# Kernel optimization log

Measured on AMD Instinct MI355X. Metric: run time of the kernel, lower is better.

Reference implementation:

```python
import jax, jax.numpy as jnp
import numpy as np
import math

EMB = 64
NEG_INF = -1e30

def _layernorm(x, g, b, eps=1e-5):
    mu = jnp.mean(x, axis=-1, keepdims=True)
    var = jnp.mean((x - mu) ** 2, axis=-1, keepdims=True)
    return (x - mu) * jax.lax.rsqrt(var + eps) * g + b

def setup_inputs() -> dict:
    key = jax.random.key(0)
    ks = jax.random.split(key, 8)
    b, t, n, d = 16, 12, 307, EMB
    s = 1.0 / math.sqrt(d)
    inp = {
        'x': jax.random.normal(ks[0], (b, t, n, d), dtype=jnp.float32),
        'stg': jax.random.uniform(ks[1], (b, n, t, n), dtype=jnp.float32),
        'topk': 3,
        'q_w': jax.random.normal(ks[2], (d, d), dtype=jnp.float32) * s,
        'q_b': jnp.zeros((d,), jnp.float32),
        'k_w': jax.random.normal(ks[3], (d, d), dtype=jnp.float32) * s,
        'k_b': jnp.zeros((d,), jnp.float32),
        'ln_g': jnp.ones((d,), jnp.float32),
        'ln_b': jnp.zeros((d,), jnp.float32),
        'ffn_ln_g': jnp.ones((d,), jnp.float32),
        'ffn_ln_b': jnp.zeros((d,), jnp.float32),
        'fc1_w': jax.random.normal(ks[4], (4 * d, d), dtype=jnp.float32) * s,
        'fc1_b': jnp.zeros((4 * d,), jnp.float32),
        'fc2_w': jax.random.normal(ks[5], (d, 4 * d), dtype=jnp.float32) * (0.5 * s),
        'fc2_b': jnp.zeros((d,), jnp.float32),
    }
    return inp

def reference(x, stg, topk, q_w, q_b, k_w, k_b, ln_g, ln_b, ffn_ln_g, ffn_ln_b, fc1_w, fc1_b, fc2_w, fc2_b):
    b, t, n, d = x.shape
    scale = 1.0 / math.sqrt(d)
    x_ = _layernorm(x, ln_g, ln_b)           # [b,t,n,d]
    y_ = x_[:, -1]                            # [b,n,d] last timestep
    q = y_ @ q_w.T + q_b                      # [b,n,d]
    k = x_ @ k_w.T + k_b                      # [b,t,n,d]
    dg = jnp.einsum('bnd,btmd->bntm', q, k) * scale
    sag = jax.nn.sigmoid(dg) * stg * scale    # gated scores [b,n,t,n]
    sag = sag.reshape(b, n, t * n)
    if topk > 0:
        kk = topk * n if topk < 5 else topk   # mirrors torch's self.topk *= n
        top_values, _ = jax.lax.top_k(sag, kk)
        thr = top_values[..., -1:]
        sag = jnp.where(sag > thr, sag, NEG_INF)  # strict >, as in torch code
    sag = jax.nn.softmax(sag, axis=-1).reshape(b, n, t, n)  # dropout in eval mode = identity
    o = jnp.einsum('bntm,btmd->bnd', sag, x_)
    h = o + y_
    # FFN: pre-norm residual MLP (LayerNorm -> Linear(d,4d) -> ReLU -> Linear(4d,d) + residual)
    z = _layernorm(h, ffn_ln_g, ffn_ln_b)
    z = jax.nn.relu(z @ fc1_w.T + fc1_b) @ fc2_w.T + fc2_b
    return h + z
```

## Files before the change

### kernel.cpp

```cpp
#include <hip/hip_runtime.h>

typedef __bf16 bf16x8 __attribute__((ext_vector_type(8)));
typedef float  f32x4  __attribute__((ext_vector_type(4)));
typedef unsigned short u16x8 __attribute__((ext_vector_type(8)));
typedef unsigned short u16x4 __attribute__((ext_vector_type(4)));

constexpr int BB    = 16;
constexpr int TT    = 12;
constexpr int NN    = 307;
constexpr int TN    = TT * NN;
constexpr int ROWSX = BB * TT * NN;
constexpr int ROWSH = BB * NN;
constexpr int SST1  = 3712;
constexpr int SSTR  = 3840;
constexpr int HPS   = ROWSH * 64;
constexpr int KQ    = 928;
constexpr int WBS   = 152;
constexpr float SCALE = 0.125f;

__device__ __forceinline__ float wred_sum(float v) {
#pragma unroll
    for (int m = 32; m > 0; m >>= 1) v += __shfl_xor(v, m, 64);
    return v;
}

__global__ __launch_bounds__(256) void prep_k(const float* __restrict__ qw,
                                              const float* __restrict__ qb,
                                              const float* __restrict__ kw,
                                              const float* __restrict__ kb,
                                              const float* __restrict__ fc1w,
                                              const float* __restrict__ fc2w,
                                              const float* __restrict__ x,
                                              const float* __restrict__ g,
                                              const float* __restrict__ b,
                                              float* __restrict__ M,
                                              float* __restrict__ b2,
                                              float* __restrict__ vv,
                                              float* __restrict__ cc,
                                              __bf16* __restrict__ fc1b16,
                                              __bf16* __restrict__ fc2b16,
                                              __bf16* __restrict__ xnb,
                                              float* __restrict__ y32) {
    int bx = blockIdx.x, t = threadIdx.x;
    int w = t >> 6, lane = t & 63;
    if (bx < 16) {
        int e = bx * 4 + w, d = lane;
        float acc = 0.f;
        for (int dp = 0; dp < 64; ++dp) acc += qw[dp * 64 + e] * kw[dp * 64 + d];
        M[e * 64 + d] = acc;
        float vp = wred_sum(qw[d * 64 + e] * kb[d]);
        if (lane == 0) vv[e] = vp;
        if (e == 0) {
            float bv = 0.f;
            for (int dp = 0; dp < 64; ++dp) bv += qb[dp] * kw[dp * 64 + d];
            b2[d] = bv;
            float cp = wred_sum(qb[d] * kb[d]);
            if (d == 0) *cc = cp;
        }
    } else if (bx < 144) {
        int i = (bx - 16) * 256 + t;
        if (i < 16384) fc1b16[i] = (__bf16)fc1w[i];
        else fc2b16[i - 16384] = (__bf16)fc2w[i - 16384];
    } else {
        int r = (bx - 144) * 4 + w;
        if (r >= ROWSX) return;
        float val = x[r * 64 + lane];
        float mu  = wred_sum(val) * (1.f / 64.f);
        float dv  = val - mu;
        float var = wred_sum(dv * dv) * (1.f / 64.f);
        float xv  = dv * rsqrtf(var + 1e-5f) * g[lane] + b[lane];
        xnb[(size_t)r * 64 + lane] = (__bf16)xv;
        int tt = (r / NN) % TT;
        if (tt == TT - 1) {
            int bbv = r / (NN * TT), n = r % NN;
            y32[(bbv * NN + n) * 64 + lane] = xv;
        }
    }
}

__global__ __launch_bounds__(256) void tq_k(const __bf16* __restrict__ xnb,
                                            __bf16* __restrict__ xnT,
                                            const float* __restrict__ y32,
                                            const float* __restrict__ M,
                                            const float* __restrict__ b2,
                                            const float* __restrict__ vv,
                                            const float* __restrict__ ccp,
                                            __bf16* __restrict__ qtb,
                                            float* __restrict__ cq) {
    __shared__ unsigned short tile[64][65];
    int bx = blockIdx.x, t = threadIdx.x;
    if (bx < 928) {
        int bb = bx / 58, j0 = (bx % 58) * 64;
        const unsigned short* src = (const unsigned short*)xnb;
        unsigned short* dst = (unsigned short*)xnT;
#pragma unroll
        for (int i = 0; i < 16; ++i) {
            int f = t + 256 * i, jr = f >> 6, dc = f & 63;
            int j = j0 + jr;
            tile[jr][dc] = (j < TN) ? src[((size_t)bb * TN + j) * 64 + dc] : (unsigned short)0;
        }
        __syncthreads();
#pragma unroll
        for (int i = 0; i < 16; ++i) {
            int f = t + 256 * i, d = f >> 6, jj = f & 63;
            dst[((size_t)bb * 64 + d) * SSTR + j0 + jj] = tile[jj][d];
        }
    } else {
        int w = t >> 6, l = t & 63;
        int rr = (bx - 928) * 4 + w;
        if (rr >= ROWSH) return;
        float y = y32[rr * 64 + l];
        float acc = b2[l];
#pragma unroll
        for (int e = 0; e < 64; ++e) acc += __shfl(y, e, 64) * M[e * 64 + l];
        qtb[(size_t)rr * 64 + l] = (__bf16)acc;
        float cp = wred_sum(y * vv[l]);
        if (l == 0) cq[rr] = cp + *ccp;
    }
}

__global__ __launch_bounds__(256, 4) void score_k(const __bf16* __restrict__ qtb,
                                                  const float* __restrict__ cq,
                                                  const __bf16* __restrict__ xnb,
                                                  const float* __restrict__ stg,
                                                  __bf16* __restrict__ sag) {
    __shared__ unsigned short wb[64 * WBS];
    int bb = blockIdx.z, n0 = blockIdx.y * 64, j0 = blockIdx.x * 128;
    int t = threadIdx.x;
    int w = t >> 6, lane = t & 63;
    int m16 = lane & 15, q4 = lane >> 4;

    const float* stgb = stg + (size_t)bb * NN * TN;
    float4 sv[4][2];
    float cn[4];
#pragma unroll
    for (int nt = 0; nt < 4; ++nt) {
        int n = n0 + nt * 16 + m16;
        const float* srow = stgb + (size_t)min(n, NN - 1) * TN;
#pragma unroll
        for (int jj = 0; jj < 2; ++jj) {
            int jb = j0 + (w * 2 + jj) * 16 + q4 * 4;
            float4 s4 = {0.f, 0.f, 0.f, 0.f};
            if (jb < TN) s4 = *(const float4*)(srow + jb);
            sv[nt][jj] = s4;
        }
        cn[nt] = (n < NN) ? cq[bb * NN + n] : 0.f;
    }

    bf16x8 a[2][2];
#pragma unroll
    for (int jj = 0; jj < 2; ++jj) {
        const bf16x8* ap = (const bf16x8*)(xnb + ((size_t)bb * TN + j0 + (w * 2 + jj) * 16 + m16) * 64);
        a[jj][0] = ap[q4];
        a[jj][1] = ap[q4 + 4];
    }

    f32x4 acc[2][4];
#pragma unroll
    for (int nt = 0; nt < 4; ++nt) {
        const bf16x8* bp = (const bf16x8*)(qtb + ((size_t)bb * NN + n0 + nt * 16 + m16) * 64);
        bf16x8 b0 = bp[q4], b1 = bp[q4 + 4];
#pragma unroll
        for (int jj = 0; jj < 2; ++jj) {
            f32x4 c = {0.f, 0.f, 0.f, 0.f};
            c = __builtin_amdgcn_mfma_f32_16x16x32_bf16(a[jj][0], b0, c, 0, 0, 0);
            c = __builtin_amdgcn_mfma_f32_16x16x32_bf16(a[jj][1], b1, c, 0, 0, 0);
            acc[jj][nt] = c;
        }
    }

#pragma unroll
    for (int nt = 0; nt < 4; ++nt) {
#pragma unroll
        for (int jj = 0; jj < 2; ++jj) {
            int jb = j0 + (w * 2 + jj) * 16 + q4 * 4;
            float svv[4] = {sv[nt][jj].x, sv[nt][jj].y, sv[nt][jj].z, sv[nt][jj].w};
            u16x4 hw;
#pragma unroll
            for (int r = 0; r < 4; ++r) {
                float dg = (acc[jj][nt][r] + cn[nt]) * SCALE;
                float s  = 1.f / (1.f + __expf(-dg));
                float wv = (jb + r < TN) ? s * svv[r] * SCALE : 0.f;
                __bf16 wb16 = (__bf16)wv;
                hw[r] = *(unsigned short*)&wb16;
            }
            *(u16x4*)&wb[(nt * 16 + m16) * WBS + (w * 2 + jj) * 16 + q4 * 4] = hw;
        }
    }
    __syncthreads();

#pragma unroll
    for (int i = 0; i < 4; ++i) {
        int chunk = t + i * 256;
        int row = chunk >> 4, c8 = (chunk & 15) * 8;
        int n = n0 + row;
        if (n < NN) {
            u16x8 v = *(const u16x8*)&wb[row * WBS + c8];
            *(u16x8*)((unsigned short*)sag + (size_t)(bb * NN + n) * SST1 + j0 + c8) = v;
        }
    }
}

__global__ __launch_bounds__(256) void smax_k(__bf16* __restrict__ sagB,
                                              const int* __restrict__ topk_p,
                                              float* __restrict__ rsum) {
    int t = threadIdx.x;
    int wid = t >> 6, lane = t & 63;
    int row = blockIdx.x * 4 + wid;
    if (row >= ROWSH) return;

    int topkv = *topk_p;
    bool selAll = (topkv <= 0);
    int kk = 0;
    if (!selAll) {
        kk = (topkv < 5) ? topkv * NN : topkv;
        if (kk > TN) kk = TN;
    }

    u16x8* src = (u16x8*)((unsigned short*)sagB + (size_t)row * SST1);
    u16x8 va[8];
#pragma unroll
    for (int ci = 0; ci < 8; ++ci) {
        int c = lane + (ci << 6);
        u16x8 v = {0, 0, 0, 0, 0, 0, 0, 0};
        if (c < 464) v = src[c];
        va[ci] = v;
    }
    int vmb = 0;
#pragma unroll
    for (int ci = 0; ci < 8; ++ci)
#pragma unroll
        for (int e = 0; e < 8; ++e) vmb = max(vmb, (int)va[ci][e]);
#pragma unroll
    for (int m = 32; m > 0; m >>= 1) vmb = max(vmb, __shfl_xor(vmb, m, 64));
    float vmax = __uint_as_float(((unsigned)vmb) << 16);

    unsigned thrb = 0;
    if (!selAll) {
        unsigned lo = 0, hi = (unsigned)vmb;
        while (lo < hi) {
            unsigned mid = (lo + hi) >> 1;
            int cnt = 0;
#pragma unroll
            for (int ci = 0; ci < 8; ++ci)
#pragma unroll
                for (int e = 0; e < 8; ++e)
                    cnt += (int)__popcll(__ballot((unsigned)va[ci][e] > mid));
            if (cnt < kk) hi = mid; else lo = mid + 1;
        }
        thrb = lo;
    }

    float local = 0.f;
#pragma unroll
    for (int ci = 0; ci < 8; ++ci) {
        int c = lane + (ci << 6);
        int nvv = (c < 460) ? 8 : ((c == 460) ? 4 : 0);
#pragma unroll
        for (int e = 0; e < 8; ++e) {
            unsigned u = va[ci][e];
            bool sel = selAll ? (e < nvv) : (u > thrb);
            float ev = sel ? __expf(__uint_as_float(u << 16) - vmax) : 0.f;
            local += ev;
            __bf16 eb = (__bf16)ev;
            va[ci][e] = *(unsigned short*)&eb;
        }
    }
    local = wred_sum(local);
    bool uni = !(local > 0.f);
    if (lane == 0) rsum[row] = uni ? (float)TN : local;

    if (uni) {
        __bf16 one = (__bf16)1.f, zero = (__bf16)0.f;
#pragma unroll
        for (int ci = 0; ci < 8; ++ci) {
            int c = lane + (ci << 6);
            if (c < 464) {
                int nvv = (c < 460) ? 8 : ((c == 460) ? 4 : 0);
                bf16x8 o;
#pragma unroll
                for (int e = 0; e < 8; ++e) o[e] = (e < nvv) ? one : zero;
                *(bf16x8*)&src[c] = o;
            }
        }
    } else {
#pragma unroll
        for (int ci = 0; ci < 8; ++ci) {
            int c = lane + (ci << 6);
            if (c < 464) src[c] = va[ci];
        }
    }
}

__global__ __launch_bounds__(256) void pv_k(const __bf16* __restrict__ sagB,
                                            const __bf16* __restrict__ xnT,
                                            const float* __restrict__ y32,
                                            const float* __restrict__ rsum,
                                            float* __restrict__ hp) {
    int bb = blockIdx.z, kq = blockIdx.y, n0 = blockIdx.x * 16;
    int wid = threadIdx.x >> 6, lane = threadIdx.x & 63;
    int m16 = lane & 15, q4 = lane >> 4;

    int arow = min(n0 + m16, NN - 1);
    const __bf16* ab  = sagB + (size_t)(bb * NN + arow) * SST1 + kq * KQ + q4 * 8;
    const __bf16* bbp = xnT + ((size_t)bb * 64 + wid * 16 + m16) * SSTR + kq * KQ + q4 * 8;

    f32x4 acc0 = {0.f, 0.f, 0.f, 0.f}, acc1 = {0.f, 0.f, 0.f, 0.f};
#pragma unroll 4
    for (int ks = 0; ks < 29; ++ks) {
        bf16x8 a = *(const bf16x8*)(ab + ks * 32);
        bf16x8 b = *(const bf16x8*)(bbp + ks * 32);
        if (ks & 1) acc1 = __builtin_amdgcn_mfma_f32_16x16x32_bf16(a, b, acc1, 0, 0, 0);
        else        acc0 = __builtin_amdgcn_mfma_f32_16x16x32_bf16(a, b, acc0, 0, 0, 0);
    }
#pragma unroll
    for (int r = 0; r < 4; ++r) {
        int n = n0 + q4 * 4 + r;
        if (n < NN) {
            size_t o = (size_t)(bb * NN + n) * 64 + wid * 16 + m16;
            float inv = 1.f / rsum[bb * NN + n];
            float v = (acc0[r] + acc1[r]) * inv;
            if (kq == 0) v += y32[o];
            hp[(size_t)kq * HPS + o] = v;
        }
    }
}

__global__ __launch_bounds__(256) void ffn_k(const float* __restrict__ hp,
                                             const float* __restrict__ g,
                                             const float* __restrict__ bln,
                                             const __bf16* __restrict__ fc1b16,
                                             const float* __restrict__ fc1b,
                                             const __bf16* __restrict__ fc2b16,
                                             const float* __restrict__ fc2b,
                                             float* __restrict__ out) {
    __shared__ __bf16 zb[16 * 68];
    __shared__ __bf16 ab[16 * 264];
    __shared__ float hs[16][66];
    int t = threadIdx.x, r0 = blockIdx.x * 16;
    int wid = t >> 6, lane = t & 63;
    int m16 = lane & 15, q4 = lane >> 4;

#pragma unroll
    for (int q = 0; q < 4; ++q) {
        int rl = wid * 4 + q;
        size_t i = (size_t)(r0 + rl) * 64 + lane;
        float val = hp[i] + hp[HPS + i] + hp[2 * HPS + i] + hp[3 * HPS + i];
        hs[rl][lane] = val;
        float mu  = wred_sum(val) * (1.f / 64.f);
        float dv  = val - mu;
        float var = wred_sum(dv * dv) * (1.f / 64.f);
        zb[rl * 68 + lane] = (__bf16)(dv * rsqrtf(var + 1e-5f) * g[lane] + bln[lane]);
    }
    __syncthreads();

    bf16x8 a0 = *(const bf16x8*)&zb[m16 * 68 + q4 * 8];
    bf16x8 a1 = *(const bf16x8*)&zb[m16 * 68 + 32 + q4 * 8];
#pragma unroll
    for (int jt2 = 0; jt2 < 4; ++jt2) {
        int j0t = (wid * 4 + jt2) * 16;
        const __bf16* bp = fc1b16 + (size_t)(j0t + m16) * 64 + q4 * 8;
        f32x4 c = {0.f, 0.f, 0.f, 0.f};
        c = __builtin_amdgcn_mfma_f32_16x16x32_bf16(a0, *(const bf16x8*)bp, c, 0, 0, 0);
        c = __builtin_amdgcn_mfma_f32_16x16x32_bf16(a1, *(const bf16x8*)(bp + 32), c, 0, 0, 0);
        int j = j0t + m16;
        float bias = fc1b[j];
#pragma unroll
        for (int r = 0; r < 4; ++r)
            ab[(q4 * 4 + r) * 264 + j] = (__bf16)fmaxf(c[r] + bias, 0.f);
    }
    __syncthreads();

    f32x4 c2a = {0.f, 0.f, 0.f, 0.f}, c2b = {0.f, 0.f, 0.f, 0.f};
    const __bf16* b2p = fc2b16 + (size_t)(wid * 16 + m16) * 256 + q4 * 8;
#pragma unroll
    for (int k8 = 0; k8 < 8; k8 += 2) {
        bf16x8 aa0 = *(const bf16x8*)&ab[m16 * 264 + k8 * 32 + q4 * 8];
        bf16x8 aa1 = *(const bf16x8*)&ab[m16 * 264 + (k8 + 1) * 32 + q4 * 8];
        c2a = __builtin_amdgcn_mfma_f32_16x16x32_bf16(aa0, *(const bf16x8*)(b2p + k8 * 32), c2a, 0, 0, 0);
        c2b = __builtin_amdgcn_mfma_f32_16x16x32_bf16(aa1, *(const bf16x8*)(b2p + (k8 + 1) * 32), c2b, 0, 0, 0);
    }
    int d = wid * 16 + m16;
    float bias2 = fc2b[d];
#pragma unroll
    for (int r = 0; r < 4; ++r) {
        size_t row = (size_t)(r0 + q4 * 4 + r);
        size_t o = row * 64 + d;
        out[o] = hs[q4 * 4 + r][d] + c2a[r] + c2b[r] + bias2;
    }
}

extern "C" void kernel_launch(void* const* d_in, const int* in_sizes, int n_in,
                              void* d_out, int out_size, void* d_ws, size_t ws_size,
                              hipStream_t stream) {
    const float* x    = (const float*)d_in[0];
    const float* stg  = (const float*)d_in[1];
    const int*   topk = (const int*)d_in[2];
    const float* qw   = (const float*)d_in[3];
    const float* qb   = (const float*)d_in[4];
    const float* kw   = (const float*)d_in[5];
    const float* kb   = (const float*)d_in[6];
    const float* lng  = (const float*)d_in[7];
    const float* lnb  = (const float*)d_in[8];
    const float* flng = (const float*)d_in[9];
    const float* flnb = (const float*)d_in[10];
    const float* fc1w = (const float*)d_in[11];
    const float* fc1b = (const float*)d_in[12];
    const float* fc2w = (const float*)d_in[13];
    const float* fc2b = (const float*)d_in[14];
    float* out = (float*)d_out;

    float* ws = (float*)d_ws;
    __bf16* xnb = (__bf16*)ws;
    float* p1   = ws + 1886208;
    __bf16* xnT = (__bf16*)p1;
    float* p2   = p1 + 1966080;
    __bf16* qtb = (__bf16*)p2;
    float* y32  = p2 + 157696;
    float* cq   = y32 + 314368;
    float* M    = cq + 4928;
    float* b2   = M + 4096;
    float* vv   = b2 + 64;
    float* cc   = vv + 64;
    __bf16* fc1b16 = (__bf16*)(cc + 16);
    __bf16* fc2b16 = (__bf16*)((float*)fc1b16 + 8192);
    __bf16* sag = (__bf16*)((float*)fc2b16 + 8192);
    float* hp   = (float*)sag + 9116672;
    float* rsum = hp + 4 * HPS;

    prep_k<<<144 + (ROWSX + 3) / 4, 256, 0, stream>>>(qw, qb, kw, kb, fc1w, fc2w,
                                                      x, lng, lnb,
                                                      M, b2, vv, cc,
                                                      fc1b16, fc2b16, xnb, y32);
    tq_k<<<928 + (ROWSH + 3) / 4, 256, 0, stream>>>(xnb, xnT, y32, M, b2, vv, cc, qtb, cq);
    score_k<<<dim3((TN + 127) / 128, (NN + 63) / 64, BB), 256, 0, stream>>>(qtb, cq, xnb, stg, sag);
    smax_k<<<(ROWSH + 3) / 4, 256, 0, stream>>>(sag, topk, rsum);
    pv_k<<<dim3((NN + 15) / 16, 4, BB), 256, 0, stream>>>(sag, xnT, y32, rsum, hp);
    ffn_k<<<ROWSH / 16, 256, 0, stream>>>(hp, flng, flnb, fc1b16, fc1b, fc2b16, fc2b, out);
}
```

Baseline: 245.8 us.

## Move transpose into score kernel and swizzle pv block order

Splits the old transpose+q kernel: the small q projection runs alone, and the xnb→xnT transpose blocks are appended to the score kernel's 1D grid so they run alongside score tiles. Separately, pv_k remaps block indices with an 8-way interleave, likely to spread batches and k-chunks across XCDs for better L2 locality. This trades a lighter serial q kernel and overlapping work against added index arithmetic and shared LDS reuse in score_k.

```diff
diff --git a/kernel.cpp b/kernel.cpp
--- a/kernel.cpp
+++ b/kernel.cpp
@@ -16,6 +16,7 @@
 constexpr int HPS   = ROWSH * 64;
 constexpr int KQ    = 928;
 constexpr int WBS   = 152;
+constexpr int SCORE_VB = 145 * BB;
 constexpr float SCALE = 0.125f;
 
 __device__ __forceinline__ float wred_sum(float v) {
@@ -78,19 +79,39 @@
     }
 }
 
-__global__ __launch_bounds__(256) void tq_k(const __bf16* __restrict__ xnb,
-                                            __bf16* __restrict__ xnT,
-                                            const float* __restrict__ y32,
+__global__ __launch_bounds__(256) void qt_k(const float* __restrict__ y32,
                                             const float* __restrict__ M,
                                             const float* __restrict__ b2,
                                             const float* __restrict__ vv,
                                             const float* __restrict__ ccp,
                                             __bf16* __restrict__ qtb,
                                             float* __restrict__ cq) {
-    __shared__ unsigned short tile[64][65];
-    int bx = blockIdx.x, t = threadIdx.x;
-    if (bx < 928) {
-        int bb = bx / 58, j0 = (bx % 58) * 64;
+    int w = threadIdx.x >> 6, l = threadIdx.x & 63;
+    int rr = blockIdx.x * 4 + w;
+    if (rr >= ROWSH) return;
+    float y = y32[rr * 64 + l];
+    float acc = b2[l];
+#pragma unroll
+    for (int e = 0; e < 64; ++e) acc += __shfl(y, e, 64) * M[e * 64 + l];
+    qtb[(size_t)rr * 64 + l] = (__bf16)acc;
+    float cp = wred_sum(y * vv[l]);
+    if (l == 0) cq[rr] = cp + *ccp;
+}
+
+__global__ __launch_bounds__(256, 4) void score_k(const __bf16* __restrict__ qtb,
+                                                  const float* __restrict__ cq,
+                                                  const __bf16* __restrict__ xnb,
+                                                  const float* __restrict__ stg,
+                                                  __bf16* __restrict__ sag,
+                                                  __bf16* __restrict__ xnT) {
+    __shared__ unsigned short wb[64 * WBS];
+    int vb = blockIdx.x;
+    int t = threadIdx.x;
+
+    if (vb >= SCORE_VB) {
+        int u = vb - SCORE_VB;
+        int bb = u / 58, j0 = (u % 58) * 64;
+        unsigned short (*tile)[65] = (unsigned short(*)[65])wb;
         const unsigned short* src = (const unsigned short*)xnb;
         unsigned short* dst = (unsigned short*)xnT;
 #pragma unroll
@@ -105,28 +126,11 @@
             int f = t + 256 * i, d = f >> 6, jj = f & 63;
             dst[((size_t)bb * 64 + d) * SSTR + j0 + jj] = tile[jj][d];
         }
-    } else {
-        int w = t >> 6, l = t & 63;
-        int rr = (bx - 928) * 4 + w;
-        if (rr >= ROWSH) return;
-        float y = y32[rr * 64 + l];
-        float acc = b2[l];
-#pragma unroll
-        for (int e = 0; e < 64; ++e) acc += __shfl(y, e, 64) * M[e * 64 + l];
-        qtb[(size_t)rr * 64 + l] = (__bf16)acc;
-        float cp = wred_sum(y * vv[l]);
-        if (l == 0) cq[rr] = cp + *ccp;
-    }
-}
-
-__global__ __launch_bounds__(256, 4) void score_k(const __bf16* __restrict__ qtb,
-                                                  const float* __restrict__ cq,
-                                                  const __bf16* __restrict__ xnb,
-                                                  const float* __restrict__ stg,
-                                                  __bf16* __restrict__ sag) {
-    __shared__ unsigned short wb[64 * WBS];
-    int bb = blockIdx.z, n0 = blockIdx.y * 64, j0 = blockIdx.x * 128;
-    int t = threadIdx.x;
+        return;
+    }
+
+    int jb = vb % 29, nb = (vb / 29) % 5, bb = vb / 145;
+    int n0 = nb * 64, j0 = jb * 128;
     int w = t >> 6, lane = t & 63;
     int m16 = lane & 15, q4 = lane >> 4;
 
@@ -139,9 +143,9 @@
         const float* srow = stgb + (size_t)min(n, NN - 1) * TN;
 #pragma unroll
         for (int jj = 0; jj < 2; ++jj) {
-            int jb = j0 + (w * 2 + jj) * 16 + q4 * 4;
+            int jb2 = j0 + (w * 2 + jj) * 16 + q4 * 4;
             float4 s4 = {0.f, 0.f, 0.f, 0.f};
-            if (jb < TN) s4 = *(const float4*)(srow + jb);
+            if (jb2 < TN) s4 = *(const float4*)(srow + jb2);
             sv[nt][jj] = s4;
         }
         cn[nt] = (n < NN) ? cq[bb * NN + n] : 0.f;
@@ -173,14 +177,14 @@
     for (int nt = 0; nt < 4; ++nt) {
 #pragma unroll
         for (int jj = 0; jj < 2; ++jj) {
-            int jb = j0 + (w * 2 + jj) * 16 + q4 * 4;
+            int jb2 = j0 + (w * 2 + jj) * 16 + q4 * 4;
             float svv[4] = {sv[nt][jj].x, sv[nt][jj].y, sv[nt][jj].z, sv[nt][jj].w};
             u16x4 hw;
 #pragma unroll
             for (int r = 0; r < 4; ++r) {
                 float dg = (acc[jj][nt][r] + cn[nt]) * SCALE;
                 float s  = 1.f / (1.f + __expf(-dg));
-                float wv = (jb + r < TN) ? s * svv[r] * SCALE : 0.f;
+                float wv = (jb2 + r < TN) ? s * svv[r] * SCALE : 0.f;
                 __bf16 wb16 = (__bf16)wv;
                 hw[r] = *(unsigned short*)&wb16;
             }
@@ -297,7 +301,11 @@
                                             const float* __restrict__ y32,
                                             const float* __restrict__ rsum,
                                             float* __restrict__ hp) {
-    int bb = blockIdx.z, kq = blockIdx.y, n0 = blockIdx.x * 16;
+    int p = blockIdx.x + 20 * (blockIdx.y + 4 * blockIdx.z);
+    int l = (p & 7) * 160 + (p >> 3);
+    int n0 = (l % 20) * 16;
+    int kq = (l / 20) & 3;
+    int bb = l / 80;
     int wid = threadIdx.x >> 6, lane = threadIdx.x & 63;
     int m16 = lane & 15, q4 = lane >> 4;
 
@@ -432,8 +440,8 @@
                                                       x, lng, lnb,
                                                       M, b2, vv, cc,
                                                       fc1b16, fc2b16, xnb, y32);
-    tq_k<<<928 + (ROWSH + 3) / 4, 256, 0, stream>>>(xnb, xnT, y32, M, b2, vv, cc, qtb, cq);
-    score_k<<<dim3((TN + 127) / 128, (NN + 63) / 64, BB), 256, 0, stream>>>(qtb, cq, xnb, stg, sag);
+    qt_k<<<(ROWSH + 3) / 4, 256, 0, stream>>>(y32, M, b2, vv, cc, qtb, cq);
+    score_k<<<SCORE_VB + 58 * BB, 256, 0, stream>>>(qtb, cq, xnb, stg, sag, xnT);
     smax_k<<<(ROWSH + 3) / 4, 256, 0, stream>>>(sag, topk, rsum);
     pv_k<<<dim3((NN + 15) / 16, 4, BB), 256, 0, stream>>>(sag, xnT, y32, rsum, hp);
     ffn_k<<<ROWSH / 16, 256, 0, stream>>>(hp, flng, flnb, fc1b16, fc1b, fc2b16, fc2b, out);
```

After: 243.0 us. No clear change (-1.1%).
